# Kernel tuning notes

Hardware: AMD Instinct MI355X
Metric: run time of the kernel (lower is better)

Reference implementation:

```python
import jax, jax.numpy as jnp
import numpy as np
import math

D_MODEL = 512
D_STATE = 16
D_CONV = 4
EXPAND = 2
D_INNER = EXPAND * D_MODEL          # 1024
D_HALF = D_INNER // 2               # 512
DT_RANK = math.ceil(D_MODEL / 16)   # 32
BATCH, SEQLEN = 2, 4096
DT_MIN, DT_MAX, DT_FLOOR = 0.001, 0.1, 1e-4


def setup_inputs() -> dict:
    key = jax.random.key(0)
    ks = jax.random.split(key, 9)

    def lin(k, fan_out, fan_in):
        return jax.random.normal(k, (fan_out, fan_in), jnp.float32) / np.float32(np.sqrt(fan_in))

    hidden_states = jax.random.normal(ks[0], (BATCH, SEQLEN, D_MODEL), jnp.float32)
    in_proj_w = lin(ks[1], D_INNER, D_MODEL)
    x_proj_w = lin(ks[2], DT_RANK + 2 * D_STATE, D_HALF)
    dt_std = np.float32(DT_RANK ** -0.5)
    dt_proj_w = jax.random.uniform(ks[3], (D_HALF, DT_RANK), jnp.float32, -dt_std, dt_std)
    dt = jnp.exp(jax.random.uniform(ks[4], (D_HALF,), jnp.float32)
                 * (math.log(DT_MAX) - math.log(DT_MIN)) + math.log(DT_MIN))
    dt = jnp.clip(dt, DT_FLOOR)
    dt_proj_b = dt + jnp.log(-jnp.expm1(-dt))  # inverse-softplus init
    A_log = jnp.log(jnp.tile(jnp.arange(1, D_STATE + 1, dtype=jnp.float32)[None, :], (D_HALF, 1)))
    D = jnp.ones((D_HALF,), jnp.float32)
    out_proj_w = lin(ks[5], D_MODEL, D_INNER)
    conv1d_x_w = jax.random.normal(ks[6], (D_HALF, 1, D_CONV), jnp.float32) / np.float32(np.sqrt(D_CONV))
    conv1d_z_w = jax.random.normal(ks[7], (D_HALF, 1, D_CONV), jnp.float32) / np.float32(np.sqrt(D_CONV))
    return dict(hidden_states=hidden_states, in_proj_w=in_proj_w,
                conv1d_x_w=conv1d_x_w, conv1d_z_w=conv1d_z_w,
                x_proj_w=x_proj_w, dt_proj_w=dt_proj_w, dt_proj_b=dt_proj_b,
                A_log=A_log, D=D, out_proj_w=out_proj_w)


def _dwconv_same(x, w):
    # x: (b, c, l); w: (c, 1, k) depthwise. torch padding='same' with k=4 pads (1, 2),
    # which matches lax 'SAME'.
    return jax.lax.conv_general_dilated(
        x, w, window_strides=(1,), padding='SAME',
        dimension_numbers=('NCH', 'OIH', 'NCH'),
        feature_group_count=x.shape[1])


def _selective_scan(x, delta, A, B, C, D):
    # x, delta: (b, d, l); A: (d, n); B, C: (b, n, l); D: (d,)
    dA = jnp.exp(jnp.einsum('bdl,dn->bldn', delta, A))        # (b, l, d, n)
    dBx = jnp.einsum('bdl,bnl,bdl->bldn', delta, B, x)        # (b, l, d, n)

    def combine(c1, c2):
        a1, b1 = c1
        a2, b2 = c2
        return a1 * a2, a2 * b1 + b2

    _, h = jax.lax.associative_scan(combine, (dA, dBx), axis=1)  # h: (b, l, d, n)
    y = jnp.einsum('bldn,bnl->bdl', h, C) + D[None, :, None] * x
    return y


def reference(hidden_states, in_proj_w, conv1d_x_w, conv1d_z_w, x_proj_w,
              dt_proj_w, dt_proj_b, A_log, D, out_proj_w):
    b, l, _ = hidden_states.shape
    xz = jnp.einsum('bld,ed->bel', hidden_states, in_proj_w)   # (b, d_inner, l)
    x, z = jnp.split(xz, 2, axis=1)                            # each (b, d_half, l)
    A = -jnp.exp(A_log.astype(jnp.float32))
    x = jax.nn.silu(_dwconv_same(x, conv1d_x_w))
    z = jax.nn.silu(_dwconv_same(z, conv1d_z_w))
    x_dbl = jnp.einsum('bdl,ed->bel', x, x_proj_w)             # (b, dt_rank+2n, l)
    dt_r = x_dbl[:, :DT_RANK]                                  # (b, dt_rank, l)
    Bm = x_dbl[:, DT_RANK:DT_RANK + D_STATE]                   # (b, n, l)
    Cm = x_dbl[:, DT_RANK + D_STATE:]                          # (b, n, l)
    dt = jnp.einsum('brl,dr->bdl', dt_r, dt_proj_w)            # (b, d_half, l)
    delta = jax.nn.softplus(dt + dt_proj_b.astype(jnp.float32)[None, :, None])
    y = _selective_scan(x, delta, A, Bm, Cm, D.astype(jnp.float32))
    y = jnp.concatenate([y, z], axis=1)                        # (b, d_inner, l)
    out = jnp.einsum('bdl,ed->ble', y, out_proj_w)             # (b, l, d_model)
    return out
```

## Files before the change

kernel.cpp:

```cpp
#include <hip/hip_runtime.h>
#include <math.h>

#define BB 2
#define LL 4096
#define DMODEL 512
#define DINNER 1024
#define DHALF 512
#define DSTATE 16
#define RK 32
#define NCH 64
#define NC 256
#define CLEN (LL/NC)
#define NG 16
#define GL (NC/NG)
#define LOG2E 1.44269504088896f

typedef __attribute__((ext_vector_type(8))) short short8;
typedef __attribute__((ext_vector_type(4))) float f32x4;

__device__ __forceinline__ float silu_f(float v) { return v / (1.f + __expf(-v)); }

__device__ __forceinline__ unsigned short f2bf(float x) {
    unsigned int u = __float_as_uint(x);
    u += 0x7fffu + ((u >> 16) & 1u);
    return (unsigned short)(u >> 16);
}
__device__ __forceinline__ float bf2f(unsigned short u) {
    return __uint_as_float((unsigned int)u << 16);
}

__device__ __forceinline__ float softplus_f(float x) {
    return fmaxf(x, 0.f) + __logf(1.f + __expf(-fabsf(x)));
}

__device__ __forceinline__ float exp2_raw(float x) { return __builtin_amdgcn_exp2f(x); }

__device__ __forceinline__ void gload16(const unsigned short* g, unsigned short* l) {
    __builtin_amdgcn_global_load_lds((const __attribute__((address_space(1))) void*)g,
                                     (__attribute__((address_space(3))) void*)l, 16, 0, 0);
}

#define H4  1048576
#define W14 131072
#define W24 131072
#define W34 8192
#define NA  8192
__global__ void cast_all(const float* __restrict__ hid, const float* __restrict__ w1,
                         const float* __restrict__ w2, const float* __restrict__ w3,
                         const float* __restrict__ A_log,
                         unsigned short* __restrict__ Hb, unsigned short* __restrict__ Wb,
                         unsigned short* __restrict__ Wob, unsigned short* __restrict__ Wxb,
                         float* __restrict__ Arow2T) {
    int i = blockIdx.x * 256 + threadIdx.x;
    if (i >= H4 + W14 + W24 + W34) {
        int j = i - (H4 + W14 + W24 + W34);
        if (j < NA) {
            int n = j >> 9, d = j & 511;
            Arow2T[j] = -expf(A_log[d * DSTATE + n]) * LOG2E;
        }
        return;
    }
    const float* src; unsigned short* dst; int j;
    if (i < H4)                    { src = hid; dst = Hb;  j = i; }
    else if (i < H4 + W14)         { src = w1;  dst = Wb;  j = i - H4; }
    else if (i < H4 + W14 + W24)   { src = w2;  dst = Wob; j = i - H4 - W14; }
    else                           { src = w3;  dst = Wxb; j = i - H4 - W14 - W24; }
    float4 v = *(const float4*)&src[(size_t)j * 4];
    ushort4 o = make_ushort4(f2bf(v.x), f2bf(v.y), f2bf(v.z), f2bf(v.w));
    *(ushort4*)&dst[(size_t)j * 4] = o;
}

template<int K, int E, bool BF16OUT>
__global__ __launch_bounds__(256, 4) void gemm_mfma(const unsigned short* __restrict__ W,
                                                    const unsigned short* __restrict__ X,
                                                    void* __restrict__ outv) {
    __shared__ unsigned short Xa[128 * 64];
    __shared__ unsigned short Wa[64 * 64];
    const int tid = threadIdx.x;
    const int lane = tid & 63;
    const int w = tid >> 6;
    const int frow = lane & 15;
    const int kg = lane >> 4;
    const int e0 = blockIdx.y * 64;
    const int r0 = blockIdx.x * 128;

    f32x4 acc[4][2] = {};

    for (int kt = 0; kt < K / 64; ++kt) {
        #pragma unroll
        for (int i = 0; i < 4; ++i) {
            int flat = i * 256 + tid;
            int row = flat >> 3;
            int slot = flat & 7;
            int chunk = slot ^ (row & 7);
            gload16(&X[(size_t)(r0 + row) * K + kt * 64 + chunk * 8], &Xa[flat * 8]);
        }
        #pragma unroll
        for (int i = 0; i < 2; ++i) {
            int flat = i * 256 + tid;
            int row = flat >> 3;
            int slot = flat & 7;
            int chunk = slot ^ (row & 7);
            gload16(&W[(size_t)(e0 + row) * K + kt * 64 + chunk * 8], &Wa[flat * 8]);
        }
        __syncthreads();

        #pragma unroll
        for (int ks = 0; ks < 2; ++ks) {
            short8 af[4], bfr[2];
            #pragma unroll
            for (int m = 0; m < 4; ++m) {
                int row = m * 16 + frow;
                int phys = (ks * 4 + kg) ^ (row & 7);
                af[m] = *(const short8*)&Wa[row * 64 + phys * 8];
            }
            #pragma unroll
            for (int n = 0; n < 2; ++n) {
                int row = w * 32 + n * 16 + frow;
                int phys = (ks * 4 + kg) ^ (row & 7);
                bfr[n] = *(const short8*)&Xa[row * 64 + phys * 8];
            }
            #pragma unroll
            for (int m = 0; m < 4; ++m)
                #pragma unroll
                for (int n = 0; n < 2; ++n)
                    acc[m][n] = __builtin_amdgcn_mfma_f32_16x16x32_bf16(af[m], bfr[n], acc[m][n], 0, 0, 0);
        }
        __syncthreads();
    }

    #pragma unroll
    for (int m = 0; m < 4; ++m) {
        #pragma unroll
        for (int n = 0; n < 2; ++n) {
            int e = e0 + m * 16 + kg * 4;
            int r = r0 + w * 32 + n * 16 + frow;
            f32x4 a = acc[m][n];
            if constexpr (BF16OUT) {
                ushort4 o = make_ushort4(f2bf(a.x), f2bf(a.y), f2bf(a.z), f2bf(a.w));
                *(ushort4*)&((unsigned short*)outv)[(size_t)r * E + e] = o;
            } else {
                *(f32x4*)&((float*)outv)[(size_t)r * E + e] = a;
            }
        }
    }
}

__global__ __launch_bounds__(256) void gemm_xproj(const unsigned short* __restrict__ W,
                                                  const unsigned short* __restrict__ X,
                                                  float* __restrict__ out) {
    __shared__ unsigned short Xa[128 * 64];
    __shared__ unsigned short Wa[64 * 64];
    const int tid = threadIdx.x;
    const int lane = tid & 63;
    const int w = tid >> 6;
    const int frow = lane & 15;
    const int kg = lane >> 4;
    const int r0 = blockIdx.x * 128;

    f32x4 acc[4][2] = {};

    for (int kt = 0; kt < 512 / 64; ++kt) {
        #pragma unroll
        for (int i = 0; i < 4; ++i) {
            int flat = i * 256 + tid;
            int row = flat >> 3;
            int slot = flat & 7;
            int chunk = slot ^ (row & 7);
            gload16(&X[(size_t)(r0 + row) * 512 + kt * 64 + chunk * 8], &Xa[flat * 8]);
        }
        #pragma unroll
        for (int i = 0; i < 2; ++i) {
            int flat = i * 256 + tid;
            int row = flat >> 3;
            int slot = flat & 7;
            int chunk = slot ^ (row & 7);
            gload16(&W[(size_t)row * 512 + kt * 64 + chunk * 8], &Wa[flat * 8]);
        }
        __syncthreads();

        #pragma unroll
        for (int ks = 0; ks < 2; ++ks) {
            short8 af[4], bfr[2];
            #pragma unroll
            for (int m = 0; m < 4; ++m) {
                int row = m * 16 + frow;
                int phys = (ks * 4 + kg) ^ (row & 7);
                af[m] = *(const short8*)&Wa[row * 64 + phys * 8];
            }
            #pragma unroll
            for (int n = 0; n < 2; ++n) {
                int row = w * 32 + n * 16 + frow;
                int phys = (ks * 4 + kg) ^ (row & 7);
                bfr[n] = *(const short8*)&Xa[row * 64 + phys * 8];
            }
            #pragma unroll
            for (int m = 0; m < 4; ++m)
                #pragma unroll
                for (int n = 0; n < 2; ++n)
                    acc[m][n] = __builtin_amdgcn_mfma_f32_16x16x32_bf16(af[m], bfr[n], acc[m][n], 0, 0, 0);
        }
        __syncthreads();
    }

    #pragma unroll
    for (int m = 0; m < 4; ++m) {
        #pragma unroll
        for (int n = 0; n < 2; ++n) {
            int r = r0 + w * 32 + n * 16 + frow;
            int b = r >> 12;
            int l = r & (LL - 1);
            int e = m * 16 + kg * 4;
            #pragma unroll
            for (int i = 0; i < 4; ++i)
                out[((size_t)b * NCH + e + i) * LL + l] = acc[m][n][i];
        }
    }
}

__global__ void conv_silu(const unsigned short* __restrict__ xzb,
                          const float* __restrict__ wx, const float* __restrict__ wz,
                          unsigned short* __restrict__ xqb, unsigned short* __restrict__ ycb) {
    __shared__ float s[67][64];
    const int b = blockIdx.z;
    const int l0 = blockIdx.x * 64;
    const int c0 = blockIdx.y * 64;
    const int tid = threadIdx.x;
    for (int idx = tid; idx < 67 * 16; idx += 256) {
        int rr = idx >> 4, u = idx & 15;
        int l = l0 - 1 + rr;
        float4 f;
        if (l >= 0 && l < LL) {
            ushort4 v = *(const ushort4*)&xzb[((size_t)b * LL + l) * DINNER + c0 + u * 4];
            f = make_float4(bf2f(v.x), bf2f(v.y), bf2f(v.z), bf2f(v.w));
        } else f = make_float4(0.f, 0.f, 0.f, 0.f);
        *(float4*)&s[rr][u * 4] = f;
    }
    __syncthreads();
    const int ct = (tid & 15) * 4;
    const int c = c0 + ct;
    const bool isx = (c < DHALF);
    const float* wp = isx ? &wx[c * 4] : &wz[(c - DHALF) * 4];
    float4 w0 = *(const float4*)&wp[0];
    float4 w1 = *(const float4*)&wp[4];
    float4 w2 = *(const float4*)&wp[8];
    float4 w3 = *(const float4*)&wp[12];
    #pragma unroll
    for (int rep = 0; rep < 4; ++rep) {
        int ll = (tid >> 4) + rep * 16;
        float4 t0 = *(const float4*)&s[ll][ct];
        float4 t1 = *(const float4*)&s[ll + 1][ct];
        float4 t2 = *(const float4*)&s[ll + 2][ct];
        float4 t3 = *(const float4*)&s[ll + 3][ct];
        float v0 = w0.x*t0.x + w0.y*t1.x + w0.z*t2.x + w0.w*t3.x;
        float v1 = w1.x*t0.y + w1.y*t1.y + w1.z*t2.y + w1.w*t3.y;
        float v2 = w2.x*t0.z + w2.y*t1.z + w2.z*t2.z + w2.w*t3.z;
        float v3 = w3.x*t0.w + w3.y*t1.w + w3.z*t2.w + w3.w*t3.w;
        ushort4 o = make_ushort4(f2bf(silu_f(v0)), f2bf(silu_f(v1)),
                                 f2bf(silu_f(v2)), f2bf(silu_f(v3)));
        int l = l0 + ll;
        if (isx) *(ushort4*)&xqb[((size_t)b * LL + l) * DHALF + c] = o;
        else     *(ushort4*)&ycb[((size_t)b * LL + l) * DINNER + c] = o;
    }
}

__global__ __launch_bounds__(256, 4) void scan1(const unsigned short* __restrict__ xqb,
                      const float* __restrict__ xdbl, const float* __restrict__ Arow2T,
                      const float* __restrict__ dtw, const float* __restrict__ dtb,
                      float* __restrict__ sdelb, float* __restrict__ delb,
                      float* __restrict__ hend) {
    __shared__ float s[48][CLEN];
    const int b = blockIdx.z;
    const int d = blockIdx.y * 256 + threadIdx.x;
    const int c = blockIdx.x;
    const int tid = threadIdx.x;
    for (int idx = tid; idx < 48 * CLEN; idx += 256) {
        int ch = idx >> 4, ll = idx & (CLEN - 1);
        s[ch][ll] = xdbl[((size_t)b * NCH + ch) * LL + c * CLEN + ll];
    }
    float dtwreg[RK];
    #pragma unroll
    for (int r = 0; r < RK; r += 4) {
        float4 v = *(const float4*)&dtw[d * RK + r];
        dtwreg[r] = v.x; dtwreg[r+1] = v.y; dtwreg[r+2] = v.z; dtwreg[r+3] = v.w;
    }
    float Arow2[DSTATE];
    #pragma unroll
    for (int n = 0; n < DSTATE; ++n) Arow2[n] = Arow2T[n * DHALF + d];
    const float bias = dtb[d];
    float del[CLEN];
    #pragma unroll
    for (int t = 0; t < CLEN; ++t) del[t] = bias;
    __syncthreads();
    #pragma unroll
    for (int r = 0; r < RK; ++r) {
        float wv = dtwreg[r];
        #pragma unroll
        for (int q = 0; q < CLEN / 4; ++q) {
            float4 v = *(const float4*)&s[r][q * 4];
            del[q*4+0] = fmaf(v.x, wv, del[q*4+0]);
            del[q*4+1] = fmaf(v.y, wv, del[q*4+1]);
            del[q*4+2] = fmaf(v.z, wv, del[q*4+2]);
            del[q*4+3] = fmaf(v.w, wv, del[q*4+3]);
        }
    }
    float sdel = 0.f;
    #pragma unroll
    for (int t = 0; t < CLEN; ++t) { del[t] = softplus_f(del[t]); sdel += del[t]; }
    size_t dbase = ((size_t)b * LL + c * CLEN) * DHALF + d;
    #pragma unroll
    for (int t = 0; t < CLEN; ++t) delb[dbase + (size_t)t * DHALF] = del[t];

    float h[DSTATE];
    #pragma unroll
    for (int n = 0; n < DSTATE; ++n) h[n] = 0.f;
    #pragma unroll
    for (int t = 0; t < CLEN; ++t) {
        float dl = del[t];
        float xv = bf2f(xqb[((size_t)b * LL + c * CLEN + t) * DHALF + d]);
        float dx = dl * xv;
        #pragma unroll
        for (int n = 0; n < DSTATE; ++n) {
            float dA = exp2_raw(dl * Arow2[n]);
            h[n] = fmaf(dA, h[n], dx * s[32 + n][t]);
        }
    }
    sdelb[((size_t)b * NC + c) * DHALF + d] = sdel;
    size_t base = (((size_t)b * NC + c) * DSTATE) * DHALF + d;
    #pragma unroll
    for (int n = 0; n < DSTATE; ++n)
        hend[base + (size_t)n * DHALF] = h[n];
}

__global__ void scan2a(const float* __restrict__ sdelb, float* __restrict__ hend,
                       const float* __restrict__ Arow2T,
                       float* __restrict__ gP, float* __restrict__ gH) {
    int flat = blockIdx.x * 256 + threadIdx.x;
    int d = flat & (DHALF - 1);
    int n = (flat >> 9) & (DSTATE - 1);
    int g = (flat >> 13) & (NG - 1);
    int b = flat >> 17;
    const float Arow2 = Arow2T[n * DHALF + d];
    const size_t stride = (size_t)DSTATE * DHALF;
    size_t idx = (((size_t)b * NC + g * GL) * DSTATE + n) * DHALF + d;
    size_t sidx = ((size_t)b * NC + g * GL) * DHALF + d;
    float S = 0.f, H = 0.f;
    #pragma unroll
    for (int j = 0; j < GL; ++j) {
        float sd = sdelb[sidx + (size_t)j * DHALF];
        float h = hend[idx];
        hend[idx] = H;
        H = fmaf(exp2_raw(Arow2 * sd), H, h);
        S += sd;
        idx += stride;
    }
    size_t gi = (((size_t)b * NG + g) * DSTATE + n) * DHALF + d;
    gP[gi] = exp2_raw(Arow2 * S);
    gH[gi] = H;
}

__global__ __launch_bounds__(256, 4) void scan3(const unsigned short* __restrict__ xqb,
                      const float* __restrict__ xdbl, const float* __restrict__ Arow2T,
                      const float* __restrict__ delb, const float* __restrict__ Dp,
                      const float* __restrict__ sdelb, const float* __restrict__ hend,
                      const float* __restrict__ gP, const float* __restrict__ gH,
                      unsigned short* __restrict__ ycb) {
    __shared__ float s[32][CLEN];
    const int b = blockIdx.z;
    const int d = blockIdx.y * 256 + threadIdx.x;
    const int c = blockIdx.x;
    const int tid = threadIdx.x;
    const int g = c / GL;
    for (int idx = tid; idx < 32 * CLEN; idx += 256) {
        int ch = 32 + (idx >> 4), ll = idx & (CLEN - 1);
        s[idx >> 4][ll] = xdbl[((size_t)b * NCH + ch) * LL + c * CLEN + ll];
    }
    float Arow2[DSTATE];
    #pragma unroll
    for (int n = 0; n < DSTATE; ++n) Arow2[n] = Arow2T[n * DHALF + d];

    float Hcar[DSTATE];
    #pragma unroll
    for (int n = 0; n < DSTATE; ++n) Hcar[n] = 0.f;
    for (int gp = 0; gp < g; ++gp) {
        size_t gi = (((size_t)b * NG + gp) * DSTATE) * DHALF + d;
        #pragma unroll
        for (int n = 0; n < DSTATE; ++n)
            Hcar[n] = fmaf(gP[gi + (size_t)n * DHALF], Hcar[n], gH[gi + (size_t)n * DHALF]);
    }
    float Sc = 0.f;
    for (int j = g * GL; j < c; ++j)
        Sc += sdelb[((size_t)b * NC + j) * DHALF + d];

    float h[DSTATE];
    size_t base = (((size_t)b * NC + c) * DSTATE) * DHALF + d;
    #pragma unroll
    for (int n = 0; n < DSTATE; ++n)
        h[n] = fmaf(exp2_raw(Arow2[n] * Sc), Hcar[n], hend[base + (size_t)n * DHALF]);

    float del[CLEN];
    size_t dbase = ((size_t)b * LL + c * CLEN) * DHALF + d;
    #pragma unroll
    for (int t = 0; t < CLEN; ++t) del[t] = delb[dbase + (size_t)t * DHALF];

    const float Dv = Dp[d];
    __syncthreads();
    #pragma unroll
    for (int t = 0; t < CLEN; ++t) {
        float dl = del[t];
        float xv = bf2f(xqb[((size_t)b * LL + c * CLEN + t) * DHALF + d]);
        float dx = dl * xv;
        float y = Dv * xv;
        #pragma unroll
        for (int n = 0; n < DSTATE; ++n) {
            float dA = exp2_raw(dl * Arow2[n]);
            h[n] = fmaf(dA, h[n], dx * s[n][t]);
            y = fmaf(h[n], s[16 + n][t], y);
        }
        ycb[((size_t)b * LL + c * CLEN + t) * DINNER + d] = f2bf(y);
    }
}

extern "C" void kernel_launch(void* const* d_in, const int* in_sizes, int n_in,
                              void* d_out, int out_size, void* d_ws, size_t ws_size,
                              hipStream_t stream) {
    const float* hidden     = (const float*)d_in[0];
    const float* in_proj_w  = (const float*)d_in[1];
    const float* conv_x_w   = (const float*)d_in[2];
    const float* conv_z_w   = (const float*)d_in[3];
    const float* x_proj_w   = (const float*)d_in[4];
    const float* dt_proj_w  = (const float*)d_in[5];
    const float* dt_proj_b  = (const float*)d_in[6];
    const float* A_log      = (const float*)d_in[7];
    const float* Dp         = (const float*)d_in[8];
    const float* out_proj_w = (const float*)d_in[9];
    float* out = (float*)d_out;

    float* ws_f = (float*)d_ws;
    unsigned short* Wb  = (unsigned short*)(ws_f + 0);
    unsigned short* Wob = (unsigned short*)(ws_f + 262144);
    unsigned short* Wxb = (unsigned short*)(ws_f + 524288);
    unsigned short* Hb  = (unsigned short*)(ws_f + 540672);
    unsigned short* xzb = (unsigned short*)(ws_f + 2637824);
    unsigned short* xqb = (unsigned short*)(ws_f + 6832128);
    unsigned short* ycb = (unsigned short*)(ws_f + 8929280);
    float* xdbl = ws_f + 13123584;
    float* gP   = ws_f + 13647872;
    float* gH   = ws_f + 13910016;
    float* Arow2T = ws_f + 14172160;
    float* delb = ws_f + 14180352;
    float* sdel = ws_f + 540672;
    float* hend = ws_f + 2637824;

    dim3 blk(256);

    cast_all<<<dim3((H4 + W14 + W24 + W34 + NA + 255) / 256), blk, 0, stream>>>(
        hidden, in_proj_w, out_proj_w, x_proj_w, A_log, Hb, Wb, Wob, Wxb, Arow2T);
    gemm_mfma<DMODEL, DINNER, true><<<dim3(BB * LL / 128, DINNER / 64), blk, 0, stream>>>(Wb, Hb, xzb);
    conv_silu<<<dim3(LL / 64, DINNER / 64, BB), blk, 0, stream>>>(xzb, conv_x_w, conv_z_w, xqb, ycb);
    gemm_xproj<<<dim3(BB * LL / 128), blk, 0, stream>>>(Wxb, xqb, xdbl);
    scan1<<<dim3(NC, DHALF / 256, BB), blk, 0, stream>>>(xqb, xdbl, Arow2T, dt_proj_w, dt_proj_b,
                                                         sdel, delb, hend);
    scan2a<<<dim3(BB * NG * DSTATE * DHALF / 256), blk, 0, stream>>>(sdel, hend, Arow2T, gP, gH);
    scan3<<<dim3(NC, DHALF / 256, BB), blk, 0, stream>>>(xqb, xdbl, Arow2T, delb, Dp,
                                                         sdel, hend, gP, gH, ycb);
    gemm_mfma<DINNER, DMODEL, false><<<dim3(BB * LL / 128, DMODEL / 64), blk, 0, stream>>>(Wob, ycb, out);
}
```

Measured before the change: 127.5 us.

## Fuse fp32-to-bf16 casts into GEMM tile loads and drop cast kernel

Removes the standalone cast_all kernel. The GEMMs now read fp32 activations and weights straight from global memory and convert them to bf16 while staging each tile into LDS. The A-matrix precompute moves into one block of conv_silu, and the workspace layout is compacted. This saves a kernel launch and a full fp32 read plus bf16 write/read round trip of the hidden states. In exchange, each GEMM tile load now costs twice the global bytes, weights are re-converted by every block, and the async global_load_lds path is replaced by register staging.

```diff
diff --git a/kernel.cpp b/kernel.cpp
--- a/kernel.cpp
+++ b/kernel.cpp
@@ -40,39 +40,18 @@
                                      (__attribute__((address_space(3))) void*)l, 16, 0, 0);
 }
 
-#define H4  1048576
-#define W14 131072
-#define W24 131072
-#define W34 8192
-#define NA  8192
-__global__ void cast_all(const float* __restrict__ hid, const float* __restrict__ w1,
-                         const float* __restrict__ w2, const float* __restrict__ w3,
-                         const float* __restrict__ A_log,
-                         unsigned short* __restrict__ Hb, unsigned short* __restrict__ Wb,
-                         unsigned short* __restrict__ Wob, unsigned short* __restrict__ Wxb,
-                         float* __restrict__ Arow2T) {
-    int i = blockIdx.x * 256 + threadIdx.x;
-    if (i >= H4 + W14 + W24 + W34) {
-        int j = i - (H4 + W14 + W24 + W34);
-        if (j < NA) {
-            int n = j >> 9, d = j & 511;
-            Arow2T[j] = -expf(A_log[d * DSTATE + n]) * LOG2E;
-        }
-        return;
-    }
-    const float* src; unsigned short* dst; int j;
-    if (i < H4)                    { src = hid; dst = Hb;  j = i; }
-    else if (i < H4 + W14)         { src = w1;  dst = Wb;  j = i - H4; }
-    else if (i < H4 + W14 + W24)   { src = w2;  dst = Wob; j = i - H4 - W14; }
-    else                           { src = w3;  dst = Wxb; j = i - H4 - W14 - W24; }
-    float4 v = *(const float4*)&src[(size_t)j * 4];
-    ushort4 o = make_ushort4(f2bf(v.x), f2bf(v.y), f2bf(v.z), f2bf(v.w));
-    *(ushort4*)&dst[(size_t)j * 4] = o;
-}
-
-template<int K, int E, bool BF16OUT>
-__global__ __launch_bounds__(256, 4) void gemm_mfma(const unsigned short* __restrict__ W,
-                                                    const unsigned short* __restrict__ X,
+__device__ __forceinline__ short8 pack_bf8(float4 a, float4 b) {
+    short8 v;
+    v[0] = (short)f2bf(a.x); v[1] = (short)f2bf(a.y);
+    v[2] = (short)f2bf(a.z); v[3] = (short)f2bf(a.w);
+    v[4] = (short)f2bf(b.x); v[5] = (short)f2bf(b.y);
+    v[6] = (short)f2bf(b.z); v[7] = (short)f2bf(b.w);
+    return v;
+}
+
+template<int K, int E, bool XF32, bool BF16OUT>
+__global__ __launch_bounds__(256, 4) void gemm_mfma(const float* __restrict__ Wf,
+                                                    const void* __restrict__ Xp,
                                                     void* __restrict__ outv) {
     __shared__ unsigned short Xa[128 * 64];
     __shared__ unsigned short Wa[64 * 64];
@@ -87,21 +66,38 @@
     f32x4 acc[4][2] = {};
 
     for (int kt = 0; kt < K / 64; ++kt) {
-        #pragma unroll
-        for (int i = 0; i < 4; ++i) {
-            int flat = i * 256 + tid;
-            int row = flat >> 3;
-            int slot = flat & 7;
-            int chunk = slot ^ (row & 7);
-            gload16(&X[(size_t)(r0 + row) * K + kt * 64 + chunk * 8], &Xa[flat * 8]);
+        if constexpr (XF32) {
+            const float* X32 = (const float*)Xp;
+            #pragma unroll
+            for (int i = 0; i < 4; ++i) {
+                int flat = i * 256 + tid;
+                int row = flat >> 3;
+                int slot = flat & 7;
+                const float* src = &X32[(size_t)(r0 + row) * K + kt * 64 + slot * 8];
+                float4 a = *(const float4*)src;
+                float4 b = *(const float4*)(src + 4);
+                *(short8*)&Xa[row * 64 + (slot ^ (row & 7)) * 8] = pack_bf8(a, b);
+            }
+        } else {
+            const unsigned short* X16 = (const unsigned short*)Xp;
+            #pragma unroll
+            for (int i = 0; i < 4; ++i) {
+                int flat = i * 256 + tid;
+                int row = flat >> 3;
+                int slot = flat & 7;
+                int chunk = slot ^ (row & 7);
+                gload16(&X16[(size_t)(r0 + row) * K + kt * 64 + chunk * 8], &Xa[flat * 8]);
+            }
         }
         #pragma unroll
         for (int i = 0; i < 2; ++i) {
             int flat = i * 256 + tid;
             int row = flat >> 3;
             int slot = flat & 7;
-            int chunk = slot ^ (row & 7);
-            gload16(&W[(size_t)(e0 + row) * K + kt * 64 + chunk * 8], &Wa[flat * 8]);
+            const float* src = &Wf[(size_t)(e0 + row) * K + kt * 64 + slot * 8];
+            float4 a = *(const float4*)src;
+            float4 b = *(const float4*)(src + 4);
+            *(short8*)&Wa[row * 64 + (slot ^ (row & 7)) * 8] = pack_bf8(a, b);
         }
         __syncthreads();
 
@@ -146,7 +142,7 @@
     }
 }
 
-__global__ __launch_bounds__(256) void gemm_xproj(const unsigned short* __restrict__ W,
+__global__ __launch_bounds__(256) void gemm_xproj(const float* __restrict__ Wf,
                                                   const unsigned short* __restrict__ X,
                                                   float* __restrict__ out) {
     __shared__ unsigned short Xa[128 * 64];
@@ -174,8 +170,10 @@
             int flat = i * 256 + tid;
             int row = flat >> 3;
             int slot = flat & 7;
-            int chunk = slot ^ (row & 7);
-            gload16(&W[(size_t)row * 512 + kt * 64 + chunk * 8], &Wa[flat * 8]);
+            const float* src = &Wf[(size_t)row * 512 + kt * 64 + slot * 8];
+            float4 a = *(const float4*)src;
+            float4 b = *(const float4*)(src + 4);
+            *(short8*)&Wa[row * 64 + (slot ^ (row & 7)) * 8] = pack_bf8(a, b);
         }
         __syncthreads();
 
@@ -220,7 +218,9 @@
 
 __global__ void conv_silu(const unsigned short* __restrict__ xzb,
                           const float* __restrict__ wx, const float* __restrict__ wz,
-                          unsigned short* __restrict__ xqb, unsigned short* __restrict__ ycb) {
+                          const float* __restrict__ A_log,
+                          unsigned short* __restrict__ xqb, unsigned short* __restrict__ ycb,
+                          float* __restrict__ Arow2T) {
     __shared__ float s[67][64];
     const int b = blockIdx.z;
     const int l0 = blockIdx.x * 64;
@@ -262,6 +262,12 @@
         if (isx) *(ushort4*)&xqb[((size_t)b * LL + l) * DHALF + c] = o;
         else     *(ushort4*)&ycb[((size_t)b * LL + l) * DINNER + c] = o;
     }
+    if (blockIdx.x == 0 && blockIdx.y == 0 && b == 0) {
+        for (int j = tid; j < DSTATE * DHALF; j += 256) {
+            int n = j >> 9, d = j & 511;
+            Arow2T[j] = -expf(A_log[d * DSTATE + n]) * LOG2E;
+        }
+    }
 }
 
 __global__ __launch_bounds__(256, 4) void scan1(const unsigned short* __restrict__ xqb,
@@ -437,32 +443,29 @@
     float* out = (float*)d_out;
 
     float* ws_f = (float*)d_ws;
-    unsigned short* Wb  = (unsigned short*)(ws_f + 0);
-    unsigned short* Wob = (unsigned short*)(ws_f + 262144);
-    unsigned short* Wxb = (unsigned short*)(ws_f + 524288);
-    unsigned short* Hb  = (unsigned short*)(ws_f + 540672);
-    unsigned short* xzb = (unsigned short*)(ws_f + 2637824);
-    unsigned short* xqb = (unsigned short*)(ws_f + 6832128);
-    unsigned short* ycb = (unsigned short*)(ws_f + 8929280);
-    float* xdbl = ws_f + 13123584;
-    float* gP   = ws_f + 13647872;
-    float* gH   = ws_f + 13910016;
-    float* Arow2T = ws_f + 14172160;
-    float* delb = ws_f + 14180352;
-    float* sdel = ws_f + 540672;
-    float* hend = ws_f + 2637824;
+    unsigned short* xzb = (unsigned short*)(ws_f + 0);
+    unsigned short* xqb = (unsigned short*)(ws_f + 4194304);
+    unsigned short* ycb = (unsigned short*)(ws_f + 6291456);
+    float* xdbl   = ws_f + 10485760;
+    float* gP     = ws_f + 11010048;
+    float* gH     = ws_f + 11272192;
+    float* Arow2T = ws_f + 11534336;
+    float* delb   = ws_f + 11542528;
+    float* sdel   = ws_f + 15736832;
+    float* hend = ws_f + 0;
 
     dim3 blk(256);
 
-    cast_all<<<dim3((H4 + W14 + W24 + W34 + NA + 255) / 256), blk, 0, stream>>>(
-        hidden, in_proj_w, out_proj_w, x_proj_w, A_log, Hb, Wb, Wob, Wxb, Arow2T);
-    gemm_mfma<DMODEL, DINNER, true><<<dim3(BB * LL / 128, DINNER / 64), blk, 0, stream>>>(Wb, Hb, xzb);
-    conv_silu<<<dim3(LL / 64, DINNER / 64, BB), blk, 0, stream>>>(xzb, conv_x_w, conv_z_w, xqb, ycb);
-    gemm_xproj<<<dim3(BB * LL / 128), blk, 0, stream>>>(Wxb, xqb, xdbl);
+    gemm_mfma<DMODEL, DINNER, true, true><<<dim3(BB * LL / 128, DINNER / 64), blk, 0, stream>>>(
+        in_proj_w, hidden, xzb);
+    conv_silu<<<dim3(LL / 64, DINNER / 64, BB), blk, 0, stream>>>(
+        xzb, conv_x_w, conv_z_w, A_log, xqb, ycb, Arow2T);
+    gemm_xproj<<<dim3(BB * LL / 128), blk, 0, stream>>>(x_proj_w, xqb, xdbl);
     scan1<<<dim3(NC, DHALF / 256, BB), blk, 0, stream>>>(xqb, xdbl, Arow2T, dt_proj_w, dt_proj_b,
                                                          sdel, delb, hend);
     scan2a<<<dim3(BB * NG * DSTATE * DHALF / 256), blk, 0, stream>>>(sdel, hend, Arow2T, gP, gH);
     scan3<<<dim3(NC, DHALF / 256, BB), blk, 0, stream>>>(xqb, xdbl, Arow2T, delb, Dp,
                                                          sdel, hend, gP, gH, ycb);
-    gemm_mfma<DINNER, DMODEL, false><<<dim3(BB * LL / 128, DMODEL / 64), blk, 0, stream>>>(Wob, ycb, out);
-}
+    gemm_mfma<DINNER, DMODEL, false, false><<<dim3(BB * LL / 128, DMODEL / 64), blk, 0, stream>>>(
+        out_proj_w, ycb, out);
+}
```

Measured after the change: 137.5 us. 1.08x slower.
